# Kernel tuning notes

Measured on AMD Instinct MI355X. Metric: run time of the kernel, lower is better.

The kernel has to match this reference:

```python
import jax, jax.numpy as jnp
import numpy as np
from jax import lax

B, N, S, D1, D2 = 16, 4096, 1024, 128, 256
C_IN, C_MID, C_OUT = D1 + D2, 256, 128
BN_EPS = 1e-5


def setup_inputs() -> dict:
    key = jax.random.key(0)
    ks = jax.random.split(key, 12)
    return {
        "xyz1": jax.random.normal(ks[0], (B, N, 3), jnp.float32),
        "xyz2": jax.random.normal(ks[1], (B, S, 3), jnp.float32),
        "points1": jax.random.normal(ks[2], (B, N, D1), jnp.float32),
        "points2": jax.random.normal(ks[3], (B, S, D2), jnp.float32),
        # 1x1 Conv1d weights (kernel size 1 -> plain channel matmul)
        "W1": jax.random.normal(ks[4], (C_MID, C_IN), jnp.float32) * (1.0 / np.sqrt(C_IN)),
        "b1": jax.random.normal(ks[5], (C_MID,), jnp.float32) * 0.01,
        "g1": jnp.ones((C_MID,), jnp.float32),
        "be1": jnp.zeros((C_MID,), jnp.float32),
        "W2": jax.random.normal(ks[6], (C_OUT, C_MID), jnp.float32) * (1.0 / np.sqrt(C_MID)),
        "b2": jax.random.normal(ks[7], (C_OUT,), jnp.float32) * 0.01,
        "g2": jnp.ones((C_OUT,), jnp.float32),
        "be2": jnp.zeros((C_OUT,), jnp.float32),
    }


def _bn_relu(x, g, be):
    # BatchNorm1d in training mode: batch stats over (B, L) per channel, biased var
    mean = jnp.mean(x, axis=(0, 2), keepdims=True)
    var = jnp.var(x, axis=(0, 2), keepdims=True)
    y = (x - mean) * lax.rsqrt(var + BN_EPS)
    return jax.nn.relu(y * g[None, :, None] + be[None, :, None])


def reference(xyz1, xyz2, points1, points2, W1, b1, g1, be1, W2, b2, g2, be2):
    # squared pairwise distances [B,N,S] via ||a||^2 - 2ab + ||b||^2
    dist = (
        jnp.sum(xyz1 * xyz1, -1)[:, :, None]
        - 2.0 * jnp.einsum("bnd,bsd->bns", xyz1, xyz2)
        + jnp.sum(xyz2 * xyz2, -1)[:, None, :]
    )
    neg_d3, idx = lax.top_k(-dist, 3)            # 3 nearest neighbors
    d3 = -neg_d3                                  # [B,N,3]
    w = 1.0 / (d3 + 1e-8)
    w = w / jnp.sum(w, -1, keepdims=True)
    gathered = jax.vmap(lambda p, i: p[i])(points2, idx)   # [B,N,3,D2]
    interp = jnp.sum(gathered * w[..., None], axis=2)      # [B,N,D2]
    new_points = jnp.concatenate([points1, interp], axis=-1)  # [B,N,D1+D2]
    x = jnp.transpose(new_points, (0, 2, 1))                   # [B,C,N]
    x = _bn_relu(jnp.einsum("oc,bcn->bon", W1, x) + b1[None, :, None], g1, be1)
    x = _bn_relu(jnp.einsum("oc,bcn->bon", W2, x) + b2[None, :, None], g2, be2)
    return jnp.transpose(x, (0, 2, 1))                         # [B,N,C_OUT]
```

## Files before the change

kernel.cpp:

```cpp
#include <hip/hip_runtime.h>
#include <hip/hip_bf16.h>

#define NB    16
#define NPT   4096
#define NSRC  1024
#define ND1   128
#define ND2   256
#define NCIN  384
#define NCMID 256
#define NCOUT 128
#define BNTOT (NB * NPT)
#define BN_EPS 1e-5f

typedef float f32x4 __attribute__((ext_vector_type(4)));
typedef short bf16x8 __attribute__((ext_vector_type(8)));
typedef unsigned int uint;

union PK8 { unsigned short u[8]; uint4 q; };
union PK4 { unsigned short u[4]; uint2 q; };

static __device__ __forceinline__ unsigned short f2bf(float f) {
  __hip_bfloat16 h = __float2bfloat16(f);
  return __builtin_bit_cast(unsigned short, h);
}
static __device__ __forceinline__ float bf2f(unsigned short u) {
  return __builtin_bit_cast(float, (uint)u << 16);
}
static __device__ __forceinline__ void gl_lds16(const unsigned short* g, unsigned short* l) {
  __builtin_amdgcn_global_load_lds(
      (const __attribute__((address_space(1))) uint*)(const void*)g,
      (__attribute__((address_space(3))) uint*)(void*)l,
      16, 0, 0);
}

#if __has_builtin(__builtin_amdgcn_fmed3f)
#define MED3F(a, b, c) __builtin_amdgcn_fmed3f((a), (b), (c))
#else
#define MED3F(a, b, c) fmaxf((a), fminf((b), (c)))
#endif

static __device__ __forceinline__ bool prec(float da, int ia, float db, int ib) {
  return (da < db) || (da == db && ia < ib);
}

#define INSV(t0, t1, t2, j0, j1, j2, d, idx)                                   \
  {                                                                            \
    const bool c0 = (d) < t0;                                                  \
    const bool c1 = (d) < t1;                                                  \
    const bool c2 = (d) < t2;                                                  \
    const float m1 = MED3F(t0, t1, (d));                                       \
    const float m2 = fminf(t2, fmaxf(t1, (d)));                                \
    t0 = fminf(t0, (d));                                                       \
    j2 = c2 ? (c1 ? j1 : (idx)) : j2;                                          \
    j1 = c1 ? (c0 ? j0 : (idx)) : j1;                                          \
    j0 = c0 ? (idx) : j0;                                                      \
    t1 = m1; t2 = m2;                                                          \
  }

#define MERGE3(d0, j0, d1, j1, d2, j2, e0, i0, e1, i1, e2, i2)                 \
  {                                                                            \
    const bool p0 = prec(d0, j0, e0, i0);                                      \
    const float l0d = p0 ? e0 : d0; const int l0j = p0 ? i0 : j0;              \
    const float r0d = p0 ? d0 : e0; const int r0j = p0 ? j0 : i0;              \
    const bool p1 = prec(d1, j1, e1, i1);                                      \
    const float w1d = p1 ? d1 : e1; const int w1j = p1 ? j1 : i1;              \
    const bool pr1 = prec(l0d, l0j, w1d, w1j);                                 \
    const float r1d = pr1 ? l0d : w1d; const int r1j = pr1 ? l0j : w1j;        \
    const float q1d = pr1 ? w1d : l0d; const int q1j = pr1 ? w1j : l0j;        \
    const bool p2 = prec(d2, j2, e2, i2);                                      \
    const float w2d = p2 ? d2 : e2; const int w2j = p2 ? j2 : i2;              \
    const bool pr2 = prec(q1d, q1j, w2d, w2j);                                 \
    const float r2d = pr2 ? q1d : w2d; const int r2j = pr2 ? q1j : w2j;        \
    d0 = r0d; j0 = r0j; d1 = r1d; j1 = r1j; d2 = r2d; j2 = r2j;                \
  }

__global__ __launch_bounds__(256) void front_kernel(
    const float* __restrict__ xyz1, const float* __restrict__ xyz2,
    const float* __restrict__ points1, const float* __restrict__ points2,
    unsigned short* __restrict__ Xbf)
{
  __shared__ float4 s2t[8 * 129];
  __shared__ int   sj[32][3];
  __shared__ float sw[32][3];
  const int tid = threadIdx.x;
  const int ptBase = blockIdx.x * 32;
  const int b = ptBase >> 12;

  {
    const float* src = xyz2 + (size_t)b * NSRC * 3 + tid * 12;
    const float4 l0 = ((const float4*)src)[0];
    const float4 l1 = ((const float4*)src)[1];
    const float4 l2 = ((const float4*)src)[2];
    const float xs[4] = {l0.x, l0.w, l1.z, l2.y};
    const float ys[4] = {l0.y, l1.x, l1.w, l2.z};
    const float zs[4] = {l0.z, l1.y, l2.x, l2.w};
#pragma unroll
    for (int u = 0; u < 4; ++u) {
      const int s = tid * 4 + u;
      const float c = xs[u] * xs[u] + ys[u] * ys[u] + zs[u] * zs[u];
      float4 v;
      v.x = -2.0f * xs[u]; v.y = -2.0f * ys[u]; v.z = -2.0f * zs[u]; v.w = c;
      s2t[(s >> 7) * 129 + (s & 127)] = v;
    }
  }

  const int ptl = tid >> 3;
  const int q = tid & 7;
  const int p = ptBase + ptl;

  {
    const int c16 = q * 16;
    const float* src = points1 + (size_t)p * ND1 + c16;
    const float4 v0 = ((const float4*)src)[0];
    const float4 v1 = ((const float4*)src)[1];
    const float4 v2 = ((const float4*)src)[2];
    const float4 v3 = ((const float4*)src)[3];
    PK8 pk;
    pk.u[0] = f2bf(v0.x); pk.u[1] = f2bf(v0.y); pk.u[2] = f2bf(v0.z); pk.u[3] = f2bf(v0.w);
    pk.u[4] = f2bf(v1.x); pk.u[5] = f2bf(v1.y); pk.u[6] = f2bf(v1.z); pk.u[7] = f2bf(v1.w);
    *(uint4*)(Xbf + (size_t)p * NCIN + c16) = pk.q;
    pk.u[0] = f2bf(v2.x); pk.u[1] = f2bf(v2.y); pk.u[2] = f2bf(v2.z); pk.u[3] = f2bf(v2.w);
    pk.u[4] = f2bf(v3.x); pk.u[5] = f2bf(v3.y); pk.u[6] = f2bf(v3.z); pk.u[7] = f2bf(v3.w);
    *(uint4*)(Xbf + (size_t)p * NCIN + c16 + 8) = pk.q;
  }
  __syncthreads();

  const float ax = xyz1[(size_t)p * 3 + 0];
  const float ay = xyz1[(size_t)p * 3 + 1];
  const float az = xyz1[(size_t)p * 3 + 2];
  const float a2 = ax * ax + ay * ay + az * az;
  const float4* slab = &s2t[q * 129];
  const int qbase = q * 128;

  const float INF = 3.4e38f;
  float ta0 = INF, ta1 = INF, ta2 = INF; int ja0 = 0, ja1 = 0, ja2 = 0;
  float tb0 = INF, tb1 = INF, tb2 = INF; int jb0 = 0, jb1 = 0, jb2 = 0;

  for (int i = 0; i < 128; i += 2) {
    const float4 va = slab[i];
    float da = va.w + a2;
    da = fmaf(va.x, ax, da); da = fmaf(va.y, ay, da); da = fmaf(va.z, az, da);
    INSV(ta0, ta1, ta2, ja0, ja1, ja2, da, qbase + i);
    const float4 vb = slab[i + 1];
    float db = vb.w + a2;
    db = fmaf(vb.x, ax, db); db = fmaf(vb.y, ay, db); db = fmaf(vb.z, az, db);
    INSV(tb0, tb1, tb2, jb0, jb1, jb2, db, qbase + i + 1);
  }
  MERGE3(ta0, ja0, ta1, ja1, ta2, ja2, tb0, jb0, tb1, jb1, tb2, jb2);

#pragma unroll
  for (int m = 1; m <= 4; m <<= 1) {
    float e0 = __shfl_xor(ta0, m), e1 = __shfl_xor(ta1, m), e2 = __shfl_xor(ta2, m);
    int i0 = __shfl_xor(ja0, m), i1 = __shfl_xor(ja1, m), i2 = __shfl_xor(ja2, m);
    MERGE3(ta0, ja0, ta1, ja1, ta2, ja2, e0, i0, e1, i1, e2, i2);
  }

  if (q == 0) {
    float w0 = 1.f / (ta0 + 1e-8f), w1 = 1.f / (ta1 + 1e-8f), w2 = 1.f / (ta2 + 1e-8f);
    const float inv = 1.f / (w0 + w1 + w2);
    sj[ptl][0] = ja0; sj[ptl][1] = ja1; sj[ptl][2] = ja2;
    sw[ptl][0] = w0 * inv; sw[ptl][1] = w1 * inv; sw[ptl][2] = w2 * inv;
  }
  __syncthreads();

  {
    const int j0 = sj[ptl][0], j1 = sj[ptl][1], j2 = sj[ptl][2];
    const float w0 = sw[ptl][0], w1 = sw[ptl][1], w2 = sw[ptl][2];
    const float* p2 = points2 + (size_t)b * NSRC * ND2;
    const int c32 = q * 32;
    const float4* r0 = (const float4*)(p2 + (size_t)j0 * ND2 + c32);
    const float4* r1 = (const float4*)(p2 + (size_t)j1 * ND2 + c32);
    const float4* r2 = (const float4*)(p2 + (size_t)j2 * ND2 + c32);
#pragma unroll
    for (int g = 0; g < 4; ++g) {
      PK8 pk;
#pragma unroll
      for (int h = 0; h < 2; ++h) {
        const float4 va = r0[g * 2 + h], vb = r1[g * 2 + h], vc = r2[g * 2 + h];
        pk.u[h * 4 + 0] = f2bf(w0 * va.x + w1 * vb.x + w2 * vc.x);
        pk.u[h * 4 + 1] = f2bf(w0 * va.y + w1 * vb.y + w2 * vc.y);
        pk.u[h * 4 + 2] = f2bf(w0 * va.z + w1 * vb.z + w2 * vc.z);
        pk.u[h * 4 + 3] = f2bf(w0 * va.w + w1 * vb.w + w2 * vc.w);
      }
      *(uint4*)(Xbf + (size_t)p * NCIN + ND1 + c32 + g * 8) = pk.q;
    }
  }
}

__global__ __launch_bounds__(256) void prep_w_kernel(
    const float* __restrict__ w1, const float* __restrict__ w2,
    unsigned short* __restrict__ w1b, unsigned short* __restrict__ w2b)
{
  const int i = blockIdx.x * 256 + threadIdx.x;
  const bool isW1 = i < 24576;
  const float4 v = isW1 ? ((const float4*)w1)[i] : ((const float4*)w2)[i - 24576];
  PK4 pk;
  pk.u[0] = f2bf(v.x); pk.u[1] = f2bf(v.y); pk.u[2] = f2bf(v.z); pk.u[3] = f2bf(v.w);
  if (isW1) ((uint2*)w1b)[i] = pk.q;
  else      ((uint2*)w2b)[i - 24576] = pk.q;
}

__global__ __launch_bounds__(256, 2) void gemm1_kernel(
    const unsigned short* __restrict__ Xbf, const unsigned short* __restrict__ W1bf,
    const float* __restrict__ bias1, unsigned short* __restrict__ h1bf,
    float* __restrict__ sum1, float* __restrict__ sq1)
{
  __shared__ unsigned short sA[2][128][32];
  __shared__ unsigned short sB[2][256][32];
  const int tid = threadIdx.x;
  const int lane = tid & 63;
  const int wave = tid >> 6;
  const int ptBase = blockIdx.x * 128;

  f32x4 acc[2][16];
#pragma unroll
  for (int m = 0; m < 2; ++m)
#pragma unroll
    for (int j = 0; j < 16; ++j)
#pragma unroll
      for (int q = 0; q < 4; ++q) acc[m][j][q] = 0.0f;

  const int fr = lane & 15;
  const int cs = lane >> 4;
  const int rdsh = ((cs ^ ((fr >> 1) & 3)) << 3);

  auto stage = [&](int buf, int kt) {
    const int k0 = kt * 32;
#pragma unroll
    for (int c = 0; c < 2; ++c) {
      const int s = c * 256 + wave * 64 + lane;
      const int row = s >> 2, c16 = s & 3;
      const int ks = c16 ^ ((row >> 1) & 3);
      gl_lds16(Xbf + (size_t)(ptBase + row) * NCIN + k0 + ks * 8,
               &sA[buf][0][0] + (c * 256 + wave * 64) * 8);
    }
#pragma unroll
    for (int c = 0; c < 4; ++c) {
      const int s = c * 256 + wave * 64 + lane;
      const int row = s >> 2, c16 = s & 3;
      const int ks = c16 ^ ((row >> 1) & 3);
      gl_lds16(W1bf + (size_t)row * NCIN + k0 + ks * 8,
               &sB[buf][0][0] + (c * 256 + wave * 64) * 8);
    }
  };

  stage(0, 0);
  __syncthreads();
  int cur = 0;
  for (int kt = 0; kt < 12; ++kt) {
    if (kt < 11) stage(cur ^ 1, kt + 1);
    const bf16x8 a0 = *(const bf16x8*)&sA[cur][wave * 32 + fr][rdsh];
    const bf16x8 a1 = *(const bf16x8*)&sA[cur][wave * 32 + 16 + fr][rdsh];
#pragma unroll
    for (int j = 0; j < 16; ++j) {
      const bf16x8 b = *(const bf16x8*)&sB[cur][j * 16 + fr][rdsh];
      acc[0][j] = __builtin_amdgcn_mfma_f32_16x16x32_bf16(a0, b, acc[0][j], 0, 0, 0);
      acc[1][j] = __builtin_amdgcn_mfma_f32_16x16x32_bf16(a1, b, acc[1][j], 0, 0, 0);
    }
    __syncthreads();
    cur ^= 1;
  }

  float* redS = (float*)&sA[0][0][0];
  float* redQ = redS + 1024;
  const int col = fr;
  const int r0 = cs * 4;
#pragma unroll
  for (int j = 0; j < 16; ++j) {
    const int ch = j * 16 + col;
    const float bb = bias1[ch];
    float s = 0.f, s2 = 0.f;
#pragma unroll
    for (int m = 0; m < 2; ++m)
#pragma unroll
      for (int q = 0; q < 4; ++q) {
        const int pt = ptBase + wave * 32 + m * 16 + r0 + q;
        const float v = acc[m][j][q] + bb;
        h1bf[(size_t)pt * NCMID + ch] = f2bf(v);
        s += v; s2 += v * v;
      }
    s += __shfl_xor(s, 16);  s2 += __shfl_xor(s2, 16);
    s += __shfl_xor(s, 32);  s2 += __shfl_xor(s2, 32);
    if (cs == 0) { redS[wave * 256 + fr * 16 + j] = s; redQ[wave * 256 + fr * 16 + j] = s2; }
  }
  __syncthreads();
  {
    const int ch = tid;
    const int f = ch & 15, j = ch >> 4;
    float s = 0.f, s2 = 0.f;
#pragma unroll
    for (int w = 0; w < 4; ++w) {
      s  += redS[w * 256 + f * 16 + j];
      s2 += redQ[w * 256 + f * 16 + j];
    }
    atomicAdd(&sum1[ch], s);
    atomicAdd(&sq1[ch], s2);
  }
}

template <int C>
__global__ void stats_kernel(const float* __restrict__ sum, const float* __restrict__ sumsq,
                             const float* __restrict__ g, const float* __restrict__ be,
                             float* __restrict__ a, float* __restrict__ d)
{
  const int c = threadIdx.x;
  const float mean = sum[c] * (1.0f / BNTOT);
  const float var = sumsq[c] * (1.0f / BNTOT) - mean * mean;
  const float inv = rsqrtf(var + BN_EPS);
  const float ac = g[c] * inv;
  a[c] = ac;
  d[c] = be[c] - mean * ac;
}

__global__ __launch_bounds__(256, 2) void gemm2_kernel(
    const unsigned short* __restrict__ h1bf, const unsigned short* __restrict__ W2bf,
    const float* __restrict__ bias2, const float* __restrict__ aff_a,
    const float* __restrict__ aff_d, unsigned short* __restrict__ h2bf,
    float* __restrict__ sum2, float* __restrict__ sq2)
{
  __shared__ unsigned short sA[2][128][32];
  __shared__ unsigned short sB[2][128][32];
  __shared__ float sa[NCMID], sd[NCMID];
  const int tid = threadIdx.x;
  const int lane = tid & 63;
  const int wave = tid >> 6;
  const int ptBase = blockIdx.x * 128;
  sa[tid] = aff_a[tid];
  sd[tid] = aff_d[tid];

  f32x4 acc[2][8];
#pragma unroll
  for (int m = 0; m < 2; ++m)
#pragma unroll
    for (int j = 0; j < 8; ++j)
#pragma unroll
      for (int q = 0; q < 4; ++q) acc[m][j][q] = 0.0f;

  const int fr = lane & 15;
  const int cs = lane >> 4;
  const int rdsh = ((cs ^ ((fr >> 1) & 3)) << 3);

  auto stageB = [&](int buf, int kt) {
    const int k0 = kt * 32;
#pragma unroll
    for (int c = 0; c < 2; ++c) {
      const int s = c * 256 + wave * 64 + lane;
      const int row = s >> 2, c16 = s & 3;
      const int ks = c16 ^ ((row >> 1) & 3);
      gl_lds16(W2bf + (size_t)row * NCMID + k0 + ks * 8,
               &sB[buf][0][0] + (c * 256 + wave * 64) * 8);
    }
  };
  auto stageA = [&](int buf, int kt) {
    const int k0 = kt * 32;
#pragma unroll
    for (int c = 0; c < 2; ++c) {
      const int s = c * 256 + tid;
      const int row = s >> 2, c16 = s & 3;
      const int ks = c16 ^ ((row >> 1) & 3);
      const int k = k0 + ks * 8;
      PK8 v;
      v.q = *(const uint4*)(h1bf + (size_t)(ptBase + row) * NCMID + k);
      PK8 pk;
#pragma unroll
      for (int j = 0; j < 8; ++j)
        pk.u[j] = f2bf(fmaxf(0.f, sa[k + j] * bf2f(v.u[j]) + sd[k + j]));
      *(uint4*)(&sA[buf][0][0] + s * 8) = pk.q;
    }
  };

  stageB(0, 0);
  __syncthreads();
  stageA(0, 0);
  __syncthreads();
  int cur = 0;
  for (int kt = 0; kt < 8; ++kt) {
    if (kt < 7) { stageB(cur ^ 1, kt + 1); stageA(cur ^ 1, kt + 1); }
    const bf16x8 a0 = *(const bf16x8*)&sA[cur][wave * 32 + fr][rdsh];
    const bf16x8 a1 = *(const bf16x8*)&sA[cur][wave * 32 + 16 + fr][rdsh];
#pragma unroll
    for (int j = 0; j < 8; ++j) {
      const bf16x8 b = *(const bf16x8*)&sB[cur][j * 16 + fr][rdsh];
      acc[0][j] = __builtin_amdgcn_mfma_f32_16x16x32_bf16(a0, b, acc[0][j], 0, 0, 0);
      acc[1][j] = __builtin_amdgcn_mfma_f32_16x16x32_bf16(a1, b, acc[1][j], 0, 0, 0);
    }
    __syncthreads();
    cur ^= 1;
  }

  float* redS = (float*)&sA[0][0][0];
  float* redQ = redS + 512;
  const int col = fr;
  const int r0 = cs * 4;
#pragma unroll
  for (int j = 0; j < 8; ++j) {
    const int ch = j * 16 + col;
    const float bb = bias2[ch];
    float s = 0.f, s2 = 0.f;
#pragma unroll
    for (int m = 0; m < 2; ++m)
#pragma unroll
      for (int q = 0; q < 4; ++q) {
        const int pt = ptBase + wave * 32 + m * 16 + r0 + q;
        const float v = acc[m][j][q] + bb;
        h2bf[(size_t)pt * NCOUT + ch] = f2bf(v);
        s += v; s2 += v * v;
      }
    s += __shfl_xor(s, 16);  s2 += __shfl_xor(s2, 16);
    s += __shfl_xor(s, 32);  s2 += __shfl_xor(s2, 32);
    if (cs == 0) { redS[wave * 128 + fr * 8 + j] = s; redQ[wave * 128 + fr * 8 + j] = s2; }
  }
  __syncthreads();
  if (tid < NCOUT) {
    const int ch = tid;
    const int f = ch & 15, j = ch >> 4;
    float s = 0.f, s2 = 0.f;
#pragma unroll
    for (int w = 0; w < 4; ++w) {
      s  += redS[w * 128 + f * 8 + j];
      s2 += redQ[w * 128 + f * 8 + j];
    }
    atomicAdd(&sum2[ch], s);
    atomicAdd(&sq2[ch], s2);
  }
}

__global__ __launch_bounds__(256) void final_kernel(
    const unsigned short* __restrict__ h2bf, float* __restrict__ out,
    const float* __restrict__ a2, const float* __restrict__ d2)
{
  __shared__ float sa[NCOUT], sd[NCOUT];
  if (threadIdx.x < NCOUT) { sa[threadIdx.x] = a2[threadIdx.x]; sd[threadIdx.x] = d2[threadIdx.x]; }
  __syncthreads();
  const int total8 = BNTOT * NCOUT / 8;
  for (int i = blockIdx.x * blockDim.x + threadIdx.x; i < total8;
       i += gridDim.x * blockDim.x) {
    PK8 v; v.q = ((const uint4*)h2bf)[i];
    const int c = (i & 15) * 8;
    float4 o0, o1;
    o0.x = fmaxf(0.f, sa[c + 0] * bf2f(v.u[0]) + sd[c + 0]);
    o0.y = fmaxf(0.f, sa[c + 1] * bf2f(v.u[1]) + sd[c + 1]);
    o0.z = fmaxf(0.f, sa[c + 2] * bf2f(v.u[2]) + sd[c + 2]);
    o0.w = fmaxf(0.f, sa[c + 3] * bf2f(v.u[3]) + sd[c + 3]);
    o1.x = fmaxf(0.f, sa[c + 4] * bf2f(v.u[4]) + sd[c + 4]);
    o1.y = fmaxf(0.f, sa[c + 5] * bf2f(v.u[5]) + sd[c + 5]);
    o1.z = fmaxf(0.f, sa[c + 6] * bf2f(v.u[6]) + sd[c + 6]);
    o1.w = fmaxf(0.f, sa[c + 7] * bf2f(v.u[7]) + sd[c + 7]);
    ((float4*)out)[i * 2]     = o0;
    ((float4*)out)[i * 2 + 1] = o1;
  }
}

extern "C" void kernel_launch(void* const* d_in, const int* in_sizes, int n_in,
                              void* d_out, int out_size, void* d_ws, size_t ws_size,
                              hipStream_t stream) {
  const float* xyz1    = (const float*)d_in[0];
  const float* xyz2    = (const float*)d_in[1];
  const float* points1 = (const float*)d_in[2];
  const float* points2 = (const float*)d_in[3];
  const float* W1      = (const float*)d_in[4];
  const float* b1      = (const float*)d_in[5];
  const float* g1      = (const float*)d_in[6];
  const float* be1     = (const float*)d_in[7];
  const float* W2      = (const float*)d_in[8];
  const float* b2      = (const float*)d_in[9];
  const float* g2      = (const float*)d_in[10];
  const float* be2     = (const float*)d_in[11];
  float* out = (float*)d_out;

  char* ws = (char*)d_ws;
  const size_t xbf_bytes = (size_t)BNTOT * NCIN * 2;
  const size_t h1_bytes  = (size_t)BNTOT * NCMID * 2;
  const size_t h2_bytes  = (size_t)BNTOT * NCOUT * 2;
  const size_t w1b_bytes = (size_t)NCMID * NCIN * 2;
  const size_t w2b_bytes = (size_t)NCOUT * NCMID * 2;
  unsigned short* Xbf  = (unsigned short*)ws;
  unsigned short* h1bf = (unsigned short*)(ws + xbf_bytes);
  unsigned short* h2bf = (unsigned short*)(ws + xbf_bytes + h1_bytes);
  unsigned short* W1bf = (unsigned short*)(ws + xbf_bytes + h1_bytes + h2_bytes);
  unsigned short* W2bf = (unsigned short*)(ws + xbf_bytes + h1_bytes + h2_bytes + w1b_bytes);
  float* stats = (float*)(ws + xbf_bytes + h1_bytes + h2_bytes + w1b_bytes + w2b_bytes);
  float* sum1 = stats;
  float* sq1  = stats + 256;
  float* sum2 = stats + 512;
  float* sq2  = stats + 640;
  float* a1   = stats + 768;
  float* dd1  = stats + 1024;
  float* a2v  = stats + 1280;
  float* dd2v = stats + 1408;

  hipMemsetAsync(stats, 0, 768 * sizeof(float), stream);

  prep_w_kernel<<<128, 256, 0, stream>>>(W1, W2, W1bf, W2bf);
  front_kernel<<<BNTOT / 32, 256, 0, stream>>>(xyz1, xyz2, points1, points2, Xbf);
  gemm1_kernel<<<BNTOT / 128, 256, 0, stream>>>(Xbf, W1bf, b1, h1bf, sum1, sq1);
  stats_kernel<NCMID><<<1, NCMID, 0, stream>>>(sum1, sq1, g1, be1, a1, dd1);
  gemm2_kernel<<<BNTOT / 128, 256, 0, stream>>>(h1bf, W2bf, b2, a1, dd1, h2bf, sum2, sq2);
  stats_kernel<NCOUT><<<1, NCOUT, 0, stream>>>(sum2, sq2, g2, be2, a2v, dd2v);
  final_kernel<<<2048, 256, 0, stream>>>(h2bf, out, a2v, dd2v);
}
```

Before: 150.5 us.

## Fuse kNN interpolation front stage into first GEMM, dropping Xbf intermediate

Merges the 3-NN search, interpolation and bf16 conversion into the first GEMM kernel. The A tile is now built on the fly from points1 and from weighted gathers of points2, so the 50MB bf16 concatenated buffer is never written or read back through HBM. Blocks grow to 512 threads, each wave now covers 16 rows instead of 32, and every thread scans 256 sources instead of 128. The cost is gather latency inside the GEMM main loop (the A staging is now synchronous global loads with conversion) and less B-fragment reuse per wave.

```diff
diff --git a/kernel.cpp b/kernel.cpp
--- a/kernel.cpp
+++ b/kernel.cpp
@@ -74,119 +74,6 @@
     d0 = r0d; j0 = r0j; d1 = r1d; j1 = r1j; d2 = r2d; j2 = r2j;                \
   }
 
-__global__ __launch_bounds__(256) void front_kernel(
-    const float* __restrict__ xyz1, const float* __restrict__ xyz2,
-    const float* __restrict__ points1, const float* __restrict__ points2,
-    unsigned short* __restrict__ Xbf)
-{
-  __shared__ float4 s2t[8 * 129];
-  __shared__ int   sj[32][3];
-  __shared__ float sw[32][3];
-  const int tid = threadIdx.x;
-  const int ptBase = blockIdx.x * 32;
-  const int b = ptBase >> 12;
-
-  {
-    const float* src = xyz2 + (size_t)b * NSRC * 3 + tid * 12;
-    const float4 l0 = ((const float4*)src)[0];
-    const float4 l1 = ((const float4*)src)[1];
-    const float4 l2 = ((const float4*)src)[2];
-    const float xs[4] = {l0.x, l0.w, l1.z, l2.y};
-    const float ys[4] = {l0.y, l1.x, l1.w, l2.z};
-    const float zs[4] = {l0.z, l1.y, l2.x, l2.w};
-#pragma unroll
-    for (int u = 0; u < 4; ++u) {
-      const int s = tid * 4 + u;
-      const float c = xs[u] * xs[u] + ys[u] * ys[u] + zs[u] * zs[u];
-      float4 v;
-      v.x = -2.0f * xs[u]; v.y = -2.0f * ys[u]; v.z = -2.0f * zs[u]; v.w = c;
-      s2t[(s >> 7) * 129 + (s & 127)] = v;
-    }
-  }
-
-  const int ptl = tid >> 3;
-  const int q = tid & 7;
-  const int p = ptBase + ptl;
-
-  {
-    const int c16 = q * 16;
-    const float* src = points1 + (size_t)p * ND1 + c16;
-    const float4 v0 = ((const float4*)src)[0];
-    const float4 v1 = ((const float4*)src)[1];
-    const float4 v2 = ((const float4*)src)[2];
-    const float4 v3 = ((const float4*)src)[3];
-    PK8 pk;
-    pk.u[0] = f2bf(v0.x); pk.u[1] = f2bf(v0.y); pk.u[2] = f2bf(v0.z); pk.u[3] = f2bf(v0.w);
-    pk.u[4] = f2bf(v1.x); pk.u[5] = f2bf(v1.y); pk.u[6] = f2bf(v1.z); pk.u[7] = f2bf(v1.w);
-    *(uint4*)(Xbf + (size_t)p * NCIN + c16) = pk.q;
-    pk.u[0] = f2bf(v2.x); pk.u[1] = f2bf(v2.y); pk.u[2] = f2bf(v2.z); pk.u[3] = f2bf(v2.w);
-    pk.u[4] = f2bf(v3.x); pk.u[5] = f2bf(v3.y); pk.u[6] = f2bf(v3.z); pk.u[7] = f2bf(v3.w);
-    *(uint4*)(Xbf + (size_t)p * NCIN + c16 + 8) = pk.q;
-  }
-  __syncthreads();
-
-  const float ax = xyz1[(size_t)p * 3 + 0];
-  const float ay = xyz1[(size_t)p * 3 + 1];
-  const float az = xyz1[(size_t)p * 3 + 2];
-  const float a2 = ax * ax + ay * ay + az * az;
-  const float4* slab = &s2t[q * 129];
-  const int qbase = q * 128;
-
-  const float INF = 3.4e38f;
-  float ta0 = INF, ta1 = INF, ta2 = INF; int ja0 = 0, ja1 = 0, ja2 = 0;
-  float tb0 = INF, tb1 = INF, tb2 = INF; int jb0 = 0, jb1 = 0, jb2 = 0;
-
-  for (int i = 0; i < 128; i += 2) {
-    const float4 va = slab[i];
-    float da = va.w + a2;
-    da = fmaf(va.x, ax, da); da = fmaf(va.y, ay, da); da = fmaf(va.z, az, da);
-    INSV(ta0, ta1, ta2, ja0, ja1, ja2, da, qbase + i);
-    const float4 vb = slab[i + 1];
-    float db = vb.w + a2;
-    db = fmaf(vb.x, ax, db); db = fmaf(vb.y, ay, db); db = fmaf(vb.z, az, db);
-    INSV(tb0, tb1, tb2, jb0, jb1, jb2, db, qbase + i + 1);
-  }
-  MERGE3(ta0, ja0, ta1, ja1, ta2, ja2, tb0, jb0, tb1, jb1, tb2, jb2);
-
-#pragma unroll
-  for (int m = 1; m <= 4; m <<= 1) {
-    float e0 = __shfl_xor(ta0, m), e1 = __shfl_xor(ta1, m), e2 = __shfl_xor(ta2, m);
-    int i0 = __shfl_xor(ja0, m), i1 = __shfl_xor(ja1, m), i2 = __shfl_xor(ja2, m);
-    MERGE3(ta0, ja0, ta1, ja1, ta2, ja2, e0, i0, e1, i1, e2, i2);
-  }
-
-  if (q == 0) {
-    float w0 = 1.f / (ta0 + 1e-8f), w1 = 1.f / (ta1 + 1e-8f), w2 = 1.f / (ta2 + 1e-8f);
-    const float inv = 1.f / (w0 + w1 + w2);
-    sj[ptl][0] = ja0; sj[ptl][1] = ja1; sj[ptl][2] = ja2;
-    sw[ptl][0] = w0 * inv; sw[ptl][1] = w1 * inv; sw[ptl][2] = w2 * inv;
-  }
-  __syncthreads();
-
-  {
-    const int j0 = sj[ptl][0], j1 = sj[ptl][1], j2 = sj[ptl][2];
-    const float w0 = sw[ptl][0], w1 = sw[ptl][1], w2 = sw[ptl][2];
-    const float* p2 = points2 + (size_t)b * NSRC * ND2;
-    const int c32 = q * 32;
-    const float4* r0 = (const float4*)(p2 + (size_t)j0 * ND2 + c32);
-    const float4* r1 = (const float4*)(p2 + (size_t)j1 * ND2 + c32);
-    const float4* r2 = (const float4*)(p2 + (size_t)j2 * ND2 + c32);
-#pragma unroll
-    for (int g = 0; g < 4; ++g) {
-      PK8 pk;
-#pragma unroll
-      for (int h = 0; h < 2; ++h) {
-        const float4 va = r0[g * 2 + h], vb = r1[g * 2 + h], vc = r2[g * 2 + h];
-        pk.u[h * 4 + 0] = f2bf(w0 * va.x + w1 * vb.x + w2 * vc.x);
-        pk.u[h * 4 + 1] = f2bf(w0 * va.y + w1 * vb.y + w2 * vc.y);
-        pk.u[h * 4 + 2] = f2bf(w0 * va.z + w1 * vb.z + w2 * vc.z);
-        pk.u[h * 4 + 3] = f2bf(w0 * va.w + w1 * vb.w + w2 * vc.w);
-      }
-      *(uint4*)(Xbf + (size_t)p * NCIN + ND1 + c32 + g * 8) = pk.q;
-    }
-  }
-}
-
 __global__ __launch_bounds__(256) void prep_w_kernel(
     const float* __restrict__ w1, const float* __restrict__ w2,
     unsigned short* __restrict__ w1b, unsigned short* __restrict__ w2b)
@@ -200,101 +87,185 @@
   else      ((uint2*)w2b)[i - 24576] = pk.q;
 }
 
-__global__ __launch_bounds__(256, 2) void gemm1_kernel(
-    const unsigned short* __restrict__ Xbf, const unsigned short* __restrict__ W1bf,
-    const float* __restrict__ bias1, unsigned short* __restrict__ h1bf,
-    float* __restrict__ sum1, float* __restrict__ sq1)
+__global__ __launch_bounds__(512, 4) void fg1_kernel(
+    const float* __restrict__ xyz1, const float* __restrict__ xyz2,
+    const float* __restrict__ points1, const float* __restrict__ points2,
+    const unsigned short* __restrict__ W1bf, const float* __restrict__ bias1,
+    unsigned short* __restrict__ h1bf, float* __restrict__ sum1, float* __restrict__ sq1)
 {
   __shared__ unsigned short sA[2][128][32];
   __shared__ unsigned short sB[2][256][32];
+  __shared__ float4 s2t[4 * 257];
+  __shared__ int   sj[128][3];
+  __shared__ float sw[128][3];
+
   const int tid = threadIdx.x;
   const int lane = tid & 63;
   const int wave = tid >> 6;
   const int ptBase = blockIdx.x * 128;
-
-  f32x4 acc[2][16];
-#pragma unroll
-  for (int m = 0; m < 2; ++m)
-#pragma unroll
-    for (int j = 0; j < 16; ++j)
-#pragma unroll
-      for (int q = 0; q < 4; ++q) acc[m][j][q] = 0.0f;
+  const int b = ptBase >> 12;
 
   const int fr = lane & 15;
   const int cs = lane >> 4;
   const int rdsh = ((cs ^ ((fr >> 1) & 3)) << 3);
 
-  auto stage = [&](int buf, int kt) {
+  auto stageB = [&](int buf, int kt) {
     const int k0 = kt * 32;
 #pragma unroll
     for (int c = 0; c < 2; ++c) {
-      const int s = c * 256 + wave * 64 + lane;
-      const int row = s >> 2, c16 = s & 3;
-      const int ks = c16 ^ ((row >> 1) & 3);
-      gl_lds16(Xbf + (size_t)(ptBase + row) * NCIN + k0 + ks * 8,
-               &sA[buf][0][0] + (c * 256 + wave * 64) * 8);
-    }
-#pragma unroll
-    for (int c = 0; c < 4; ++c) {
-      const int s = c * 256 + wave * 64 + lane;
+      const int base = c * 512 + wave * 64;
+      const int s = base + lane;
       const int row = s >> 2, c16 = s & 3;
       const int ks = c16 ^ ((row >> 1) & 3);
       gl_lds16(W1bf + (size_t)row * NCIN + k0 + ks * 8,
-               &sB[buf][0][0] + (c * 256 + wave * 64) * 8);
+               &sB[buf][0][0] + base * 8);
     }
   };
 
-  stage(0, 0);
-  __syncthreads();
+  auto stageA = [&](int buf, int kt) {
+    const int k0 = kt * 32;
+    const int row = tid >> 2, c16 = tid & 3;
+    const int ks = c16 ^ ((row >> 1) & 3);
+    const int k = k0 + ks * 8;
+    PK8 pk;
+    if (k < ND1) {
+      const float* src = points1 + (size_t)(ptBase + row) * ND1 + k;
+      const float4 va = ((const float4*)src)[0];
+      const float4 vb = ((const float4*)src)[1];
+      pk.u[0] = f2bf(va.x); pk.u[1] = f2bf(va.y); pk.u[2] = f2bf(va.z); pk.u[3] = f2bf(va.w);
+      pk.u[4] = f2bf(vb.x); pk.u[5] = f2bf(vb.y); pk.u[6] = f2bf(vb.z); pk.u[7] = f2bf(vb.w);
+    } else {
+      const float* p2 = points2 + (size_t)b * NSRC * ND2 + (k - ND1);
+      const int j0 = sj[row][0], j1 = sj[row][1], j2 = sj[row][2];
+      const float w0 = sw[row][0], w1 = sw[row][1], w2 = sw[row][2];
+      const float4* r0 = (const float4*)(p2 + (size_t)j0 * ND2);
+      const float4* r1 = (const float4*)(p2 + (size_t)j1 * ND2);
+      const float4* r2 = (const float4*)(p2 + (size_t)j2 * ND2);
+#pragma unroll
+      for (int h = 0; h < 2; ++h) {
+        const float4 va = r0[h], vb = r1[h], vc = r2[h];
+        pk.u[h * 4 + 0] = f2bf(w0 * va.x + w1 * vb.x + w2 * vc.x);
+        pk.u[h * 4 + 1] = f2bf(w0 * va.y + w1 * vb.y + w2 * vc.y);
+        pk.u[h * 4 + 2] = f2bf(w0 * va.z + w1 * vb.z + w2 * vc.z);
+        pk.u[h * 4 + 3] = f2bf(w0 * va.w + w1 * vb.w + w2 * vc.w);
+      }
+    }
+    *(uint4*)(&sA[buf][0][0] + tid * 8) = pk.q;
+  };
+
+  stageB(0, 0);
+  if (tid < 256) {
+    const float* src = xyz2 + (size_t)b * NSRC * 3 + tid * 12;
+    const float4 l0 = ((const float4*)src)[0];
+    const float4 l1 = ((const float4*)src)[1];
+    const float4 l2 = ((const float4*)src)[2];
+    const float xs[4] = {l0.x, l0.w, l1.z, l2.y};
+    const float ys[4] = {l0.y, l1.x, l1.w, l2.z};
+    const float zs[4] = {l0.z, l1.y, l2.x, l2.w};
+    const int qq = tid >> 6;
+    const int ibase = (tid & 63) * 4;
+#pragma unroll
+    for (int u = 0; u < 4; ++u) {
+      const float c = xs[u] * xs[u] + ys[u] * ys[u] + zs[u] * zs[u];
+      float4 v;
+      v.x = -2.0f * xs[u]; v.y = -2.0f * ys[u]; v.z = -2.0f * zs[u]; v.w = c;
+      s2t[qq * 257 + ibase + u] = v;
+    }
+  }
+  stageA(0, 0);
+  __syncthreads();
+
+  {
+    const int ptl = tid >> 2;
+    const int q = tid & 3;
+    const int p = ptBase + ptl;
+    const float ax = xyz1[(size_t)p * 3 + 0];
+    const float ay = xyz1[(size_t)p * 3 + 1];
+    const float az = xyz1[(size_t)p * 3 + 2];
+    const float a2 = ax * ax + ay * ay + az * az;
+    const float4* slab = &s2t[q * 257];
+    const int qbase = q * 256;
+
+    const float INF = 3.4e38f;
+    float ta0 = INF, ta1 = INF, ta2 = INF; int ja0 = 0, ja1 = 0, ja2 = 0;
+    float tb0 = INF, tb1 = INF, tb2 = INF; int jb0 = 0, jb1 = 0, jb2 = 0;
+
+    for (int i = 0; i < 256; i += 2) {
+      const float4 va = slab[i];
+      float da = va.w + a2;
+      da = fmaf(va.x, ax, da); da = fmaf(va.y, ay, da); da = fmaf(va.z, az, da);
+      INSV(ta0, ta1, ta2, ja0, ja1, ja2, da, qbase + i);
+      const float4 vb = slab[i + 1];
+      float db = vb.w + a2;
+      db = fmaf(vb.x, ax, db); db = fmaf(vb.y, ay, db); db = fmaf(vb.z, az, db);
+      INSV(tb0, tb1, tb2, jb0, jb1, jb2, db, qbase + i + 1);
+    }
+    MERGE3(ta0, ja0, ta1, ja1, ta2, ja2, tb0, jb0, tb1, jb1, tb2, jb2);
+
+#pragma unroll
+    for (int m = 1; m <= 2; m <<= 1) {
+      float e0 = __shfl_xor(ta0, m), e1 = __shfl_xor(ta1, m), e2 = __shfl_xor(ta2, m);
+      int i0 = __shfl_xor(ja0, m), i1 = __shfl_xor(ja1, m), i2 = __shfl_xor(ja2, m);
+      MERGE3(ta0, ja0, ta1, ja1, ta2, ja2, e0, i0, e1, i1, e2, i2);
+    }
+
+    if (q == 0) {
+      float w0 = 1.f / (ta0 + 1e-8f), w1 = 1.f / (ta1 + 1e-8f), w2 = 1.f / (ta2 + 1e-8f);
+      const float inv = 1.f / (w0 + w1 + w2);
+      sj[ptl][0] = ja0; sj[ptl][1] = ja1; sj[ptl][2] = ja2;
+      sw[ptl][0] = w0 * inv; sw[ptl][1] = w1 * inv; sw[ptl][2] = w2 * inv;
+    }
+  }
+  __syncthreads();
+
+  f32x4 acc[16];
+#pragma unroll
+  for (int j = 0; j < 16; ++j)
+#pragma unroll
+    for (int q = 0; q < 4; ++q) acc[j][q] = 0.0f;
+
   int cur = 0;
   for (int kt = 0; kt < 12; ++kt) {
-    if (kt < 11) stage(cur ^ 1, kt + 1);
-    const bf16x8 a0 = *(const bf16x8*)&sA[cur][wave * 32 + fr][rdsh];
-    const bf16x8 a1 = *(const bf16x8*)&sA[cur][wave * 32 + 16 + fr][rdsh];
+    if (kt < 11) { stageB(cur ^ 1, kt + 1); stageA(cur ^ 1, kt + 1); }
+    const bf16x8 a = *(const bf16x8*)&sA[cur][wave * 16 + fr][rdsh];
 #pragma unroll
     for (int j = 0; j < 16; ++j) {
-      const bf16x8 b = *(const bf16x8*)&sB[cur][j * 16 + fr][rdsh];
-      acc[0][j] = __builtin_amdgcn_mfma_f32_16x16x32_bf16(a0, b, acc[0][j], 0, 0, 0);
-      acc[1][j] = __builtin_amdgcn_mfma_f32_16x16x32_bf16(a1, b, acc[1][j], 0, 0, 0);
+      const bf16x8 bv = *(const bf16x8*)&sB[cur][j * 16 + fr][rdsh];
+      acc[j] = __builtin_amdgcn_mfma_f32_16x16x32_bf16(a, bv, acc[j], 0, 0, 0);
     }
     __syncthreads();
     cur ^= 1;
   }
 
   float* redS = (float*)&sA[0][0][0];
-  float* redQ = redS + 1024;
-  const int col = fr;
+  float* redQ = redS + 2048;
   const int r0 = cs * 4;
 #pragma unroll
   for (int j = 0; j < 16; ++j) {
-    const int ch = j * 16 + col;
+    const int ch = j * 16 + fr;
     const float bb = bias1[ch];
     float s = 0.f, s2 = 0.f;
 #pragma unroll
-    for (int m = 0; m < 2; ++m)
-#pragma unroll
-      for (int q = 0; q < 4; ++q) {
-        const int pt = ptBase + wave * 32 + m * 16 + r0 + q;
-        const float v = acc[m][j][q] + bb;
-        h1bf[(size_t)pt * NCMID + ch] = f2bf(v);
-        s += v; s2 += v * v;
-      }
+    for (int q = 0; q < 4; ++q) {
+      const int pt = ptBase + wave * 16 + r0 + q;
+      const float v = acc[j][q] + bb;
+      h1bf[(size_t)pt * NCMID + ch] = f2bf(v);
+      s += v; s2 += v * v;
+    }
     s += __shfl_xor(s, 16);  s2 += __shfl_xor(s2, 16);
     s += __shfl_xor(s, 32);  s2 += __shfl_xor(s2, 32);
-    if (cs == 0) { redS[wave * 256 + fr * 16 + j] = s; redQ[wave * 256 + fr * 16 + j] = s2; }
-  }
-  __syncthreads();
-  {
-    const int ch = tid;
-    const int f = ch & 15, j = ch >> 4;
+    if (cs == 0) { redS[wave * 256 + ch] = s; redQ[wave * 256 + ch] = s2; }
+  }
+  __syncthreads();
+  if (tid < NCMID) {
     float s = 0.f, s2 = 0.f;
 #pragma unroll
-    for (int w = 0; w < 4; ++w) {
-      s  += redS[w * 256 + f * 16 + j];
-      s2 += redQ[w * 256 + f * 16 + j];
-    }
-    atomicAdd(&sum1[ch], s);
-    atomicAdd(&sq1[ch], s2);
+    for (int w = 0; w < 8; ++w) {
+      s  += redS[w * 256 + tid];
+      s2 += redQ[w * 256 + tid];
+    }
+    atomicAdd(&sum1[tid], s);
+    atomicAdd(&sq1[tid], s2);
   }
 }
 
@@ -469,17 +440,15 @@
   float* out = (float*)d_out;
 
   char* ws = (char*)d_ws;
-  const size_t xbf_bytes = (size_t)BNTOT * NCIN * 2;
   const size_t h1_bytes  = (size_t)BNTOT * NCMID * 2;
   const size_t h2_bytes  = (size_t)BNTOT * NCOUT * 2;
   const size_t w1b_bytes = (size_t)NCMID * NCIN * 2;
   const size_t w2b_bytes = (size_t)NCOUT * NCMID * 2;
-  unsigned short* Xbf  = (unsigned short*)ws;
-  unsigned short* h1bf = (unsigned short*)(ws + xbf_bytes);
-  unsigned short* h2bf = (unsigned short*)(ws + xbf_bytes + h1_bytes);
-  unsigned short* W1bf = (unsigned short*)(ws + xbf_bytes + h1_bytes + h2_bytes);
-  unsigned short* W2bf = (unsigned short*)(ws + xbf_bytes + h1_bytes + h2_bytes + w1b_bytes);
-  float* stats = (float*)(ws + xbf_bytes + h1_bytes + h2_bytes + w1b_bytes + w2b_bytes);
+  unsigned short* h1bf = (unsigned short*)ws;
+  unsigned short* h2bf = (unsigned short*)(ws + h1_bytes);
+  unsigned short* W1bf = (unsigned short*)(ws + h1_bytes + h2_bytes);
+  unsigned short* W2bf = (unsigned short*)(ws + h1_bytes + h2_bytes + w1b_bytes);
+  float* stats = (float*)(ws + h1_bytes + h2_bytes + w1b_bytes + w2b_bytes);
   float* sum1 = stats;
   float* sq1  = stats + 256;
   float* sum2 = stats + 512;
@@ -492,8 +461,8 @@
   hipMemsetAsync(stats, 0, 768 * sizeof(float), stream);
 
   prep_w_kernel<<<128, 256, 0, stream>>>(W1, W2, W1bf, W2bf);
-  front_kernel<<<BNTOT / 32, 256, 0, stream>>>(xyz1, xyz2, points1, points2, Xbf);
-  gemm1_kernel<<<BNTOT / 128, 256, 0, stream>>>(Xbf, W1bf, b1, h1bf, sum1, sq1);
+  fg1_kernel<<<BNTOT / 128, 512, 0, stream>>>(xyz1, xyz2, points1, points2,
+                                              W1bf, b1, h1bf, sum1, sq1);
   stats_kernel<NCMID><<<1, NCMID, 0, stream>>>(sum1, sq1, g1, be1, a1, dd1);
   gemm2_kernel<<<BNTOT / 128, 256, 0, stream>>>(h1bf, W2bf, b2, a1, dd1, h2bf, sum2, sq2);
   stats_kernel<NCOUT><<<1, NCOUT, 0, stream>>>(sum2, sq2, g2, be2, a2v, dd2v);
```

Measured after the change: 124.5 us. 1.21x faster.

## Split fused front kernel into separate points1-cast, kNN, and interpolation kernels

Applied to the files above, without the earlier changes.

Replaces the single front kernel with three kernels: one that casts points1 to bf16, one that computes 3-NN per point (64 points per block, each wave scanning a quarter of the sources, merged through shared memory), and one that gathers and weights points2 rows into the bf16 activation buffer. Neighbor indices and weights go through a new global workspace buffer. The intent is to give each phase its own parallel mapping and raise the number of source points per block, amortizing the xyz2 shared load. The cost is extra launches and a round trip through global memory for indices and weights.

```diff
diff --git a/kernel.cpp b/kernel.cpp
--- a/kernel.cpp
+++ b/kernel.cpp
@@ -74,16 +74,44 @@
     d0 = r0d; j0 = r0j; d1 = r1d; j1 = r1j; d2 = r2d; j2 = r2j;                \
   }
 
-__global__ __launch_bounds__(256) void front_kernel(
+__global__ __launch_bounds__(256) void prep_w_kernel(
+    const float* __restrict__ w1, const float* __restrict__ w2,
+    unsigned short* __restrict__ w1b, unsigned short* __restrict__ w2b)
+{
+  const int i = blockIdx.x * 256 + threadIdx.x;
+  const bool isW1 = i < 24576;
+  const float4 v = isW1 ? ((const float4*)w1)[i] : ((const float4*)w2)[i - 24576];
+  PK4 pk;
+  pk.u[0] = f2bf(v.x); pk.u[1] = f2bf(v.y); pk.u[2] = f2bf(v.z); pk.u[3] = f2bf(v.w);
+  if (isW1) ((uint2*)w1b)[i] = pk.q;
+  else      ((uint2*)w2b)[i - 24576] = pk.q;
+}
+
+__global__ __launch_bounds__(256) void prep_x_kernel(
+    const float* __restrict__ points1, unsigned short* __restrict__ Xbf)
+{
+  const int t = blockIdx.x * 256 + threadIdx.x;
+  const int pt = t >> 4;
+  const int seg = (t & 15) * 8;
+  const float4 va = ((const float4*)(points1 + (size_t)pt * ND1 + seg))[0];
+  const float4 vb = ((const float4*)(points1 + (size_t)pt * ND1 + seg))[1];
+  PK8 pk;
+  pk.u[0] = f2bf(va.x); pk.u[1] = f2bf(va.y); pk.u[2] = f2bf(va.z); pk.u[3] = f2bf(va.w);
+  pk.u[4] = f2bf(vb.x); pk.u[5] = f2bf(vb.y); pk.u[6] = f2bf(vb.z); pk.u[7] = f2bf(vb.w);
+  *(uint4*)(Xbf + (size_t)pt * NCIN + seg) = pk.q;
+}
+
+__global__ __launch_bounds__(256) void knn_kernel(
     const float* __restrict__ xyz1, const float* __restrict__ xyz2,
-    const float* __restrict__ points1, const float* __restrict__ points2,
-    unsigned short* __restrict__ Xbf)
-{
-  __shared__ float4 s2t[8 * 129];
-  __shared__ int   sj[32][3];
-  __shared__ float sw[32][3];
+    int* __restrict__ nidx, float* __restrict__ nwgt)
+{
+  __shared__ float4 s2t[NSRC];
+  __shared__ float md[64][4][3];
+  __shared__ int   mj[64][4][3];
   const int tid = threadIdx.x;
-  const int ptBase = blockIdx.x * 32;
+  const int lane = tid & 63;
+  const int wave = tid >> 6;
+  const int ptBase = blockIdx.x * 64;
   const int b = ptBase >> 12;
 
   {
@@ -96,108 +124,81 @@
     const float zs[4] = {l0.z, l1.y, l2.x, l2.w};
 #pragma unroll
     for (int u = 0; u < 4; ++u) {
-      const int s = tid * 4 + u;
       const float c = xs[u] * xs[u] + ys[u] * ys[u] + zs[u] * zs[u];
       float4 v;
       v.x = -2.0f * xs[u]; v.y = -2.0f * ys[u]; v.z = -2.0f * zs[u]; v.w = c;
-      s2t[(s >> 7) * 129 + (s & 127)] = v;
-    }
-  }
-
-  const int ptl = tid >> 3;
-  const int q = tid & 7;
-  const int p = ptBase + ptl;
-
-  {
-    const int c16 = q * 16;
-    const float* src = points1 + (size_t)p * ND1 + c16;
-    const float4 v0 = ((const float4*)src)[0];
-    const float4 v1 = ((const float4*)src)[1];
-    const float4 v2 = ((const float4*)src)[2];
-    const float4 v3 = ((const float4*)src)[3];
-    PK8 pk;
-    pk.u[0] = f2bf(v0.x); pk.u[1] = f2bf(v0.y); pk.u[2] = f2bf(v0.z); pk.u[3] = f2bf(v0.w);
-    pk.u[4] = f2bf(v1.x); pk.u[5] = f2bf(v1.y); pk.u[6] = f2bf(v1.z); pk.u[7] = f2bf(v1.w);
-    *(uint4*)(Xbf + (size_t)p * NCIN + c16) = pk.q;
-    pk.u[0] = f2bf(v2.x); pk.u[1] = f2bf(v2.y); pk.u[2] = f2bf(v2.z); pk.u[3] = f2bf(v2.w);
-    pk.u[4] = f2bf(v3.x); pk.u[5] = f2bf(v3.y); pk.u[6] = f2bf(v3.z); pk.u[7] = f2bf(v3.w);
-    *(uint4*)(Xbf + (size_t)p * NCIN + c16 + 8) = pk.q;
-  }
-  __syncthreads();
-
+      s2t[tid * 4 + u] = v;
+    }
+  }
+  __syncthreads();
+
+  const int p = ptBase + lane;
   const float ax = xyz1[(size_t)p * 3 + 0];
   const float ay = xyz1[(size_t)p * 3 + 1];
   const float az = xyz1[(size_t)p * 3 + 2];
   const float a2 = ax * ax + ay * ay + az * az;
-  const float4* slab = &s2t[q * 129];
-  const int qbase = q * 128;
+  const float4* slab = &s2t[wave * 256];
+  const int qbase = wave * 256;
 
   const float INF = 3.4e38f;
-  float ta0 = INF, ta1 = INF, ta2 = INF; int ja0 = 0, ja1 = 0, ja2 = 0;
-  float tb0 = INF, tb1 = INF, tb2 = INF; int jb0 = 0, jb1 = 0, jb2 = 0;
-
-  for (int i = 0; i < 128; i += 2) {
-    const float4 va = slab[i];
-    float da = va.w + a2;
-    da = fmaf(va.x, ax, da); da = fmaf(va.y, ay, da); da = fmaf(va.z, az, da);
-    INSV(ta0, ta1, ta2, ja0, ja1, ja2, da, qbase + i);
-    const float4 vb = slab[i + 1];
-    float db = vb.w + a2;
-    db = fmaf(vb.x, ax, db); db = fmaf(vb.y, ay, db); db = fmaf(vb.z, az, db);
-    INSV(tb0, tb1, tb2, jb0, jb1, jb2, db, qbase + i + 1);
-  }
-  MERGE3(ta0, ja0, ta1, ja1, ta2, ja2, tb0, jb0, tb1, jb1, tb2, jb2);
-
-#pragma unroll
-  for (int m = 1; m <= 4; m <<= 1) {
-    float e0 = __shfl_xor(ta0, m), e1 = __shfl_xor(ta1, m), e2 = __shfl_xor(ta2, m);
-    int i0 = __shfl_xor(ja0, m), i1 = __shfl_xor(ja1, m), i2 = __shfl_xor(ja2, m);
-    MERGE3(ta0, ja0, ta1, ja1, ta2, ja2, e0, i0, e1, i1, e2, i2);
-  }
-
-  if (q == 0) {
-    float w0 = 1.f / (ta0 + 1e-8f), w1 = 1.f / (ta1 + 1e-8f), w2 = 1.f / (ta2 + 1e-8f);
+  float t0 = INF, t1 = INF, t2 = INF;
+  int j0 = 0, j1 = 0, j2 = 0;
+#pragma unroll 4
+  for (int i = 0; i < 256; ++i) {
+    const float4 v = slab[i];
+    float d = v.w + a2;
+    d = fmaf(v.x, ax, d); d = fmaf(v.y, ay, d); d = fmaf(v.z, az, d);
+    INSV(t0, t1, t2, j0, j1, j2, d, qbase + i);
+  }
+  md[lane][wave][0] = t0; md[lane][wave][1] = t1; md[lane][wave][2] = t2;
+  mj[lane][wave][0] = j0; mj[lane][wave][1] = j1; mj[lane][wave][2] = j2;
+  __syncthreads();
+
+  if (tid < 64) {
+    float d0 = md[tid][0][0], d1 = md[tid][0][1], d2 = md[tid][0][2];
+    int   i0 = mj[tid][0][0], i1 = mj[tid][0][1], i2 = mj[tid][0][2];
+#pragma unroll
+    for (int w = 1; w < 4; ++w) {
+      const float e0 = md[tid][w][0], e1 = md[tid][w][1], e2 = md[tid][w][2];
+      const int   k0 = mj[tid][w][0], k1 = mj[tid][w][1], k2 = mj[tid][w][2];
+      MERGE3(d0, i0, d1, i1, d2, i2, e0, k0, e1, k1, e2, k2);
+    }
+    const int pp = ptBase + tid;
+    float w0 = 1.f / (d0 + 1e-8f), w1 = 1.f / (d1 + 1e-8f), w2 = 1.f / (d2 + 1e-8f);
     const float inv = 1.f / (w0 + w1 + w2);
-    sj[ptl][0] = ja0; sj[ptl][1] = ja1; sj[ptl][2] = ja2;
-    sw[ptl][0] = w0 * inv; sw[ptl][1] = w1 * inv; sw[ptl][2] = w2 * inv;
-  }
-  __syncthreads();
-
-  {
-    const int j0 = sj[ptl][0], j1 = sj[ptl][1], j2 = sj[ptl][2];
-    const float w0 = sw[ptl][0], w1 = sw[ptl][1], w2 = sw[ptl][2];
-    const float* p2 = points2 + (size_t)b * NSRC * ND2;
-    const int c32 = q * 32;
-    const float4* r0 = (const float4*)(p2 + (size_t)j0 * ND2 + c32);
-    const float4* r1 = (const float4*)(p2 + (size_t)j1 * ND2 + c32);
-    const float4* r2 = (const float4*)(p2 + (size_t)j2 * ND2 + c32);
-#pragma unroll
-    for (int g = 0; g < 4; ++g) {
-      PK8 pk;
-#pragma unroll
-      for (int h = 0; h < 2; ++h) {
-        const float4 va = r0[g * 2 + h], vb = r1[g * 2 + h], vc = r2[g * 2 + h];
-        pk.u[h * 4 + 0] = f2bf(w0 * va.x + w1 * vb.x + w2 * vc.x);
-        pk.u[h * 4 + 1] = f2bf(w0 * va.y + w1 * vb.y + w2 * vc.y);
-        pk.u[h * 4 + 2] = f2bf(w0 * va.z + w1 * vb.z + w2 * vc.z);
-        pk.u[h * 4 + 3] = f2bf(w0 * va.w + w1 * vb.w + w2 * vc.w);
-      }
-      *(uint4*)(Xbf + (size_t)p * NCIN + ND1 + c32 + g * 8) = pk.q;
-    }
-  }
-}
-
-__global__ __launch_bounds__(256) void prep_w_kernel(
-    const float* __restrict__ w1, const float* __restrict__ w2,
-    unsigned short* __restrict__ w1b, unsigned short* __restrict__ w2b)
-{
-  const int i = blockIdx.x * 256 + threadIdx.x;
-  const bool isW1 = i < 24576;
-  const float4 v = isW1 ? ((const float4*)w1)[i] : ((const float4*)w2)[i - 24576];
-  PK4 pk;
-  pk.u[0] = f2bf(v.x); pk.u[1] = f2bf(v.y); pk.u[2] = f2bf(v.z); pk.u[3] = f2bf(v.w);
-  if (isW1) ((uint2*)w1b)[i] = pk.q;
-  else      ((uint2*)w2b)[i - 24576] = pk.q;
+    nidx[(size_t)pp * 3 + 0] = i0;
+    nidx[(size_t)pp * 3 + 1] = i1;
+    nidx[(size_t)pp * 3 + 2] = i2;
+    nwgt[(size_t)pp * 3 + 0] = w0 * inv;
+    nwgt[(size_t)pp * 3 + 1] = w1 * inv;
+    nwgt[(size_t)pp * 3 + 2] = w2 * inv;
+  }
+}
+
+__global__ __launch_bounds__(256) void interp_kernel(
+    const float* __restrict__ points2, const int* __restrict__ nidx,
+    const float* __restrict__ nwgt, unsigned short* __restrict__ Xbf)
+{
+  const int tid = threadIdx.x;
+  const int pt = blockIdx.x * 8 + (tid >> 5);
+  const int c8 = (tid & 31) * 8;
+  const int b = pt >> 12;
+  const float* p2 = points2 + (size_t)b * NSRC * ND2;
+  const int j0 = nidx[pt * 3 + 0], j1 = nidx[pt * 3 + 1], j2 = nidx[pt * 3 + 2];
+  const float w0 = nwgt[pt * 3 + 0], w1 = nwgt[pt * 3 + 1], w2 = nwgt[pt * 3 + 2];
+  const float4* r0 = (const float4*)(p2 + (size_t)j0 * ND2 + c8);
+  const float4* r1 = (const float4*)(p2 + (size_t)j1 * ND2 + c8);
+  const float4* r2 = (const float4*)(p2 + (size_t)j2 * ND2 + c8);
+  PK8 pk;
+#pragma unroll
+  for (int h = 0; h < 2; ++h) {
+    const float4 va = r0[h], vb = r1[h], vc = r2[h];
+    pk.u[h * 4 + 0] = f2bf(w0 * va.x + w1 * vb.x + w2 * vc.x);
+    pk.u[h * 4 + 1] = f2bf(w0 * va.y + w1 * vb.y + w2 * vc.y);
+    pk.u[h * 4 + 2] = f2bf(w0 * va.z + w1 * vb.z + w2 * vc.z);
+    pk.u[h * 4 + 3] = f2bf(w0 * va.w + w1 * vb.w + w2 * vc.w);
+  }
+  *(uint4*)(Xbf + (size_t)pt * NCIN + ND1 + c8) = pk.q;
 }
 
 __global__ __launch_bounds__(256, 2) void gemm1_kernel(
@@ -474,12 +475,15 @@
   const size_t h2_bytes  = (size_t)BNTOT * NCOUT * 2;
   const size_t w1b_bytes = (size_t)NCMID * NCIN * 2;
   const size_t w2b_bytes = (size_t)NCOUT * NCMID * 2;
+  const size_t idx_bytes = (size_t)BNTOT * 3 * 4;
   unsigned short* Xbf  = (unsigned short*)ws;
   unsigned short* h1bf = (unsigned short*)(ws + xbf_bytes);
   unsigned short* h2bf = (unsigned short*)(ws + xbf_bytes + h1_bytes);
   unsigned short* W1bf = (unsigned short*)(ws + xbf_bytes + h1_bytes + h2_bytes);
   unsigned short* W2bf = (unsigned short*)(ws + xbf_bytes + h1_bytes + h2_bytes + w1b_bytes);
-  float* stats = (float*)(ws + xbf_bytes + h1_bytes + h2_bytes + w1b_bytes + w2b_bytes);
+  int*   nidx = (int*)(ws + xbf_bytes + h1_bytes + h2_bytes + w1b_bytes + w2b_bytes);
+  float* nwgt = (float*)(ws + xbf_bytes + h1_bytes + h2_bytes + w1b_bytes + w2b_bytes + idx_bytes);
+  float* stats = (float*)(ws + xbf_bytes + h1_bytes + h2_bytes + w1b_bytes + w2b_bytes + 2 * idx_bytes);
   float* sum1 = stats;
   float* sq1  = stats + 256;
   float* sum2 = stats + 512;
@@ -492,7 +496,9 @@
   hipMemsetAsync(stats, 0, 768 * sizeof(float), stream);
 
   prep_w_kernel<<<128, 256, 0, stream>>>(W1, W2, W1bf, W2bf);
-  front_kernel<<<BNTOT / 32, 256, 0, stream>>>(xyz1, xyz2, points1, points2, Xbf);
+  prep_x_kernel<<<BNTOT * (ND1 / 8) / 256, 256, 0, stream>>>(points1, Xbf);
+  knn_kernel<<<BNTOT / 64, 256, 0, stream>>>(xyz1, xyz2, nidx, nwgt);
+  interp_kernel<<<BNTOT / 8, 256, 0, stream>>>(points2, nidx, nwgt, Xbf);
   gemm1_kernel<<<BNTOT / 128, 256, 0, stream>>>(Xbf, W1bf, b1, h1bf, sum1, sq1);
   stats_kernel<NCMID><<<1, NCMID, 0, stream>>>(sum1, sq1, g1, be1, a1, dd1);
   gemm2_kernel<<<BNTOT / 128, 256, 0, stream>>>(h1bf, W2bf, b2, a1, dd1, h2bf, sum2, sq2);
```

Result: no change. 149.5 us (-0.7%).
